# Kernel optimization log

Measured on AMD Instinct MI355X. Metric: run time of the kernel, lower is better.

## Reference

```python
import jax, jax.numpy as jnp
import numpy as np

D_FEAT = 6
T = 64
HID = 128
N = 8192
EPS = 1e-5


def setup_inputs() -> dict:
    key = jax.random.key(0)
    ks = jax.random.split(key, 16)
    s = 0.08
    rn = lambda k, shape: jax.random.normal(k, shape, dtype=jnp.float32) * s
    return {
        "x": jax.random.normal(ks[0], (N, D_FEAT * T), dtype=jnp.float32),
        "w_ih0": rn(ks[1], (3 * HID, D_FEAT)),
        "w_hh0": rn(ks[2], (3 * HID, HID)),
        "b_ih0": rn(ks[3], (3 * HID,)),
        "b_hh0": rn(ks[4], (3 * HID,)),
        "w_ih1": rn(ks[5], (3 * HID, HID)),
        "w_hh1": rn(ks[6], (3 * HID, HID)),
        "b_ih1": rn(ks[7], (3 * HID,)),
        "b_hh1": rn(ks[8], (3 * HID,)),
        "bn1_g": jnp.ones((HID,), jnp.float32),
        "bn1_b": jnp.zeros((HID,), jnp.float32),
        "fc_w": rn(ks[9], (HID, HID)),
        "fc_b": rn(ks[10], (HID,)),
        "bn2_g": jnp.ones((HID,), jnp.float32),
        "bn2_b": jnp.zeros((HID,), jnp.float32),
        "fco_w": rn(ks[11], (1, HID)),
        "fco_b": rn(ks[12], (1,)),
    }


def _gru_layer(xs, w_ih, w_hh, b_ih, b_hh):
    # xs: [T, N, in] -> per-step hidden states [T, N, H] (torch nn.GRU math)
    H = w_hh.shape[1]
    gi_all = jnp.einsum('tni,gi->tng', xs, w_ih) + b_ih  # precompute input gates [T,N,3H]

    def step(h, gi):
        gh = h @ w_hh.T + b_hh
        i_r, i_z, i_n = jnp.split(gi, 3, axis=1)
        h_r, h_z, h_n = jnp.split(gh, 3, axis=1)
        r = jax.nn.sigmoid(i_r + h_r)
        z = jax.nn.sigmoid(i_z + h_z)
        n = jnp.tanh(i_n + r * h_n)
        h_new = (1.0 - z) * n + z * h
        return h_new, h_new

    h0 = jnp.zeros((xs.shape[1], H), dtype=xs.dtype)
    _, hs = jax.lax.scan(step, h0, gi_all)
    return hs


def _bn(x, g, b):
    # BatchNorm1d with track_running_stats=False: always uses batch stats
    mu = jnp.mean(x, axis=0)
    var = jnp.mean((x - mu) ** 2, axis=0)
    return (x - mu) * jax.lax.rsqrt(var + EPS) * g + b


def reference(x, w_ih0, w_hh0, b_ih0, b_hh0, w_ih1, w_hh1, b_ih1, b_hh1,
              bn1_g, bn1_b, fc_w, fc_b, bn2_g, bn2_b, fco_w, fco_b):
    n = x.shape[0]
    # reshape(N, d_feat, T).permute(0,2,1) -> time-major [T, N, d_feat] for scan
    xs = x.reshape(n, D_FEAT, T).transpose(2, 0, 1)
    h1 = _gru_layer(xs, w_ih0, w_hh0, b_ih0, b_hh0)
    h2 = _gru_layer(h1, w_ih1, w_hh1, b_ih1, b_hh1)
    hidden = _bn(h2[-1], bn1_g, bn1_b)  # [N, H]
    # cal_attention: mean_d(h_i * h_j) - mean(h_i)*mean(h_j)
    #   == (hidden @ hidden.T)/H - outer(row_means, row_means)  (exact identity)
    m = jnp.mean(hidden, axis=1)
    att = hidden @ hidden.T / jnp.float32(hidden.shape[1]) - jnp.outer(m, m)  # [N, N]
    out = att @ hidden              # [N, H]
    out = out @ fc_w.T + fc_b
    out = _bn(out, bn2_g, bn2_b)
    out = jax.nn.leaky_relu(out, 0.01)
    return (out @ fco_w.T + fco_b).squeeze(-1)  # [N]
```

## Files before the change

### kernel.cpp

```cpp
#include <hip/hip_runtime.h>

typedef unsigned short u16;
typedef short bf16x8 __attribute__((ext_vector_type(8)));
typedef float f32x4 __attribute__((ext_vector_type(4)));

#define NBATCH 8192

__device__ __forceinline__ f32x4 mfma16(bf16x8 a, bf16x8 b, f32x4 c) {
  return __builtin_amdgcn_mfma_f32_16x16x32_bf16(a, b, c, 0, 0, 0);
}
__device__ __forceinline__ u16 f2bf(float f) {
  unsigned int u = __float_as_uint(f);
  return (u16)((u + 0x7FFFu + ((u >> 16) & 1u)) >> 16);
}
__device__ __forceinline__ float bf2f(u16 h) {
  return __uint_as_float(((unsigned int)h) << 16);
}
__device__ __forceinline__ float sigm(float x) {
  return __builtin_amdgcn_rcpf(1.f + __builtin_amdgcn_exp2f(-1.44269504f * x));
}
__device__ __forceinline__ float tanh_(float x) {
  float t = __builtin_amdgcn_exp2f(2.88539008f * x);
  return 1.f - 2.f * __builtin_amdgcn_rcpf(t + 1.f);
}
__device__ __forceinline__ bf16x8 pack8(const float* p) {
  float4 a = *(const float4*)p, b = *(const float4*)(p + 4);
  bf16x8 r;
  r[0] = (short)f2bf(a.x); r[1] = (short)f2bf(a.y);
  r[2] = (short)f2bf(a.z); r[3] = (short)f2bf(a.w);
  r[4] = (short)f2bf(b.x); r[5] = (short)f2bf(b.y);
  r[6] = (short)f2bf(b.z); r[7] = (short)f2bf(b.w);
  return r;
}

#define WHH0_OFF 0
#define H0B_OFF  98304
#define H1B_OFF  114688
#define XB_OFF   131072
#define GRU_LDS  135168

#define GRU_STEP(RD, WR, T)                                                     \
  {                                                                             \
    if (xact && (T) < 63) {                                                     \
      u16 xh = f2bf(xv);                                                        \
      u16 xl = f2bf(xv - bf2f(xh));                                             \
      char* xw = sm + XB_OFF + (WR)*2048 + xm*64 + xd*2;                        \
      *(u16*)xw = xh; *(u16*)(xw + 16) = xl; *(u16*)(xw + 32) = xh;             \
      if ((T) < 62) xv = gx[(T) + 2];                                           \
    }                                                                           \
    f32x4 rz0[2][2], hn0[2], in0[2];                                            \
    _Pragma("unroll") for (int mt = 0; mt < 2; ++mt) {                          \
      rz0[mt][0] = (f32x4){brz0r, brz0r, brz0r, brz0r};                         \
      rz0[mt][1] = (f32x4){brz0z, brz0z, brz0z, brz0z};                         \
      hn0[mt] = (f32x4){bhn0, bhn0, bhn0, bhn0};                                \
      in0[mt] = (f32x4){bin0, bin0, bin0, bin0};                                \
    }                                                                           \
    _Pragma("unroll") for (int ki = 0; ki < 4; ++ki) {                          \
      bf16x8 a0 = *(bf16x8*)(sm + H0B_OFF + (RD)*8192 + arow0 + ad[ki]);        \
      bf16x8 a1 = *(bf16x8*)(sm + H0B_OFF + (RD)*8192 + arow1 + ad[ki]);        \
      bf16x8 b0 = *(bf16x8*)(sm + brow0 + ad[ki]);                              \
      bf16x8 b1 = *(bf16x8*)(sm + brow1 + ad[ki]);                              \
      bf16x8 b2 = *(bf16x8*)(sm + brow2 + ad[ki]);                              \
      rz0[0][0] = mfma16(a0, b0, rz0[0][0]);                                    \
      rz0[0][1] = mfma16(a0, b1, rz0[0][1]);                                    \
      hn0[0]    = mfma16(a0, b2, hn0[0]);                                       \
      rz0[1][0] = mfma16(a1, b0, rz0[1][0]);                                    \
      rz0[1][1] = mfma16(a1, b1, rz0[1][1]);                                    \
      hn0[1]    = mfma16(a1, b2, hn0[1]);                                       \
    }                                                                           \
    {                                                                           \
      bf16x8 ax0 = *(bf16x8*)(sm + XB_OFF + (RD)*2048 + xr0);                   \
      bf16x8 ax1 = *(bf16x8*)(sm + XB_OFF + (RD)*2048 + xr1);                   \
      rz0[0][0] = mfma16(ax0, wf0a, rz0[0][0]);                                 \
      rz0[0][1] = mfma16(ax0, wf0b, rz0[0][1]);                                 \
      in0[0]    = mfma16(ax0, wf0c, in0[0]);                                    \
      rz0[1][0] = mfma16(ax1, wf0a, rz0[1][0]);                                 \
      rz0[1][1] = mfma16(ax1, wf0b, rz0[1][1]);                                 \
      in0[1]    = mfma16(ax1, wf0c, in0[1]);                                    \
    }                                                                           \
    _Pragma("unroll") for (int mt = 0; mt < 2; ++mt)                            \
    _Pragma("unroll") for (int r = 0; r < 4; ++r) {                             \
      int s = mt*4 + r;                                                         \
      float rr = sigm(rz0[mt][0][r]);                                           \
      float zz = sigm(rz0[mt][1][r]);                                           \
      float nn = tanh_(__builtin_fmaf(rr, hn0[mt][r], in0[mt][r]));             \
      float h = h0s[s]; h = __builtin_fmaf(zz, h - nn, nn); h0s[s] = h;         \
      *(u16*)(sm + H0B_OFF + (WR)*8192 + st[s]) = f2bf(h);                      \
    }                                                                           \
    __syncthreads();                                                            \
    f32x4 rz1[2][2], hn1[2], in1[2];                                            \
    _Pragma("unroll") for (int mt = 0; mt < 2; ++mt) {                          \
      rz1[mt][0] = (f32x4){brz1r, brz1r, brz1r, brz1r};                         \
      rz1[mt][1] = (f32x4){brz1z, brz1z, brz1z, brz1z};                         \
      hn1[mt] = (f32x4){bhn1, bhn1, bhn1, bhn1};                                \
      in1[mt] = (f32x4){bin1, bin1, bin1, bin1};                                \
    }                                                                           \
    _Pragma("unroll") for (int ki = 0; ki < 4; ++ki) {                          \
      bf16x8 p0 = *(bf16x8*)(sm + H0B_OFF + (WR)*8192 + arow0 + ad[ki]);        \
      bf16x8 p1 = *(bf16x8*)(sm + H0B_OFF + (WR)*8192 + arow1 + ad[ki]);        \
      bf16x8 q0 = *(bf16x8*)(sm + H1B_OFF + (RD)*8192 + arow0 + ad[ki]);        \
      bf16x8 q1 = *(bf16x8*)(sm + H1B_OFF + (RD)*8192 + arow1 + ad[ki]);        \
      rz1[0][0] = mfma16(p0, wih1f[0][ki], rz1[0][0]);                          \
      rz1[0][0] = mfma16(q0, whh1f[0][ki], rz1[0][0]);                          \
      rz1[0][1] = mfma16(p0, wih1f[1][ki], rz1[0][1]);                          \
      rz1[0][1] = mfma16(q0, whh1f[1][ki], rz1[0][1]);                          \
      in1[0]    = mfma16(p0, wih1f[2][ki], in1[0]);                             \
      hn1[0]    = mfma16(q0, whh1f[2][ki], hn1[0]);                             \
      rz1[1][0] = mfma16(p1, wih1f[0][ki], rz1[1][0]);                          \
      rz1[1][0] = mfma16(q1, whh1f[0][ki], rz1[1][0]);                          \
      rz1[1][1] = mfma16(p1, wih1f[1][ki], rz1[1][1]);                          \
      rz1[1][1] = mfma16(q1, whh1f[1][ki], rz1[1][1]);                          \
      in1[1]    = mfma16(p1, wih1f[2][ki], in1[1]);                             \
      hn1[1]    = mfma16(q1, whh1f[2][ki], hn1[1]);                             \
    }                                                                           \
    _Pragma("unroll") for (int mt = 0; mt < 2; ++mt)                            \
    _Pragma("unroll") for (int r = 0; r < 4; ++r) {                             \
      int s = mt*4 + r;                                                         \
      float rr = sigm(rz1[mt][0][r]);                                           \
      float zz = sigm(rz1[mt][1][r]);                                           \
      float nn = tanh_(__builtin_fmaf(rr, hn1[mt][r], in1[mt][r]));             \
      float h = h1s[s]; h = __builtin_fmaf(zz, h - nn, nn); h1s[s] = h;         \
      *(u16*)(sm + H1B_OFF + (WR)*8192 + st[s]) = f2bf(h);                      \
    }                                                                           \
  }

__global__ __attribute__((amdgpu_flat_work_group_size(512, 512), amdgpu_waves_per_eu(2, 2)))
void k_gru(const float* __restrict__ x,
           const float* __restrict__ wih0, const float* __restrict__ whh0,
           const float* __restrict__ bih0, const float* __restrict__ bhh0,
           const float* __restrict__ wih1, const float* __restrict__ whh1,
           const float* __restrict__ bih1, const float* __restrict__ bhh1,
           float* __restrict__ hraw) {
  extern __shared__ char sm[];
  const int tid = threadIdx.x;
  const int wid = tid >> 6;
  const int lane = tid & 63;
  const int lq = lane >> 4;
  const int ul = lane & 15;
  const int u  = wid * 16 + ul;
  const int n0 = blockIdx.x * 32;
  const int sx = (ul & 7) << 4;

  for (int idx = tid; idx < 9216; idx += 512)
    *(float*)(sm + H0B_OFF + idx * 4) = 0.f;
  for (int idx = tid; idx < 12288; idx += 512) {
    int g = idx >> 5, c4 = (idx & 31) * 4;
    float4 v = *(const float4*)(whh0 + g * 128 + c4);
    unsigned int p0 = (unsigned int)f2bf(v.x) | ((unsigned int)f2bf(v.y) << 16);
    unsigned int p1 = (unsigned int)f2bf(v.z) | ((unsigned int)f2bf(v.w) << 16);
    unsigned int* dst = (unsigned int*)(sm + WHH0_OFF + g * 256 + ((c4 * 2) ^ ((g & 7) << 4)));
    dst[0] = p0; dst[1] = p1;
  }

  bf16x8 wih1f[3][4], whh1f[3][4];
#pragma unroll
  for (int i = 0; i < 3; ++i) {
    int g = u + 128 * i;
#pragma unroll
    for (int ki = 0; ki < 4; ++ki) {
      wih1f[i][ki] = pack8(wih1 + g * 128 + ki * 32 + lq * 8);
      whh1f[i][ki] = pack8(whh1 + g * 128 + ki * 32 + lq * 8);
    }
  }
  bf16x8 wf0a, wf0b, wf0c;
  {
    u16 t0[8] = {0,0,0,0,0,0,0,0}, t1[8] = {0,0,0,0,0,0,0,0}, t2[8] = {0,0,0,0,0,0,0,0};
    u16* ts[3] = {t0, t1, t2};
#pragma unroll
    for (int i = 0; i < 3; ++i) {
      int g = u + 128 * i;
      if (lq < 2) {
        for (int d = 0; d < 6; ++d) ts[i][d] = f2bf(wih0[g * 6 + d]);
      } else if (lq == 2) {
        for (int d = 0; d < 6; ++d) {
          float w = wih0[g * 6 + d];
          u16 h = f2bf(w);
          ts[i][d] = f2bf(w - bf2f(h));
        }
      }
    }
    wf0a = *(bf16x8*)t0; wf0b = *(bf16x8*)t1; wf0c = *(bf16x8*)t2;
  }
  const float brz0r = bih0[u] + bhh0[u];
  const float brz0z = bih0[u + 128] + bhh0[u + 128];
  const float bin0 = bih0[u + 256], bhn0 = bhh0[u + 256];
  const float brz1r = bih1[u] + bhh1[u];
  const float brz1z = bih1[u + 128] + bhh1[u + 128];
  const float bin1 = bih1[u + 256], bhn1 = bhh1[u + 256];

  int ad[4];
#pragma unroll
  for (int ki = 0; ki < 4; ++ki) ad[ki] = (ki * 64 + lq * 16) ^ sx;
  const int arow0 = ul * 256, arow1 = arow0 + 4096;
  const int xr0 = ul * 64 + lq * 16, xr1 = xr0 + 1024;
  const int brow0 = WHH0_OFF + u * 256;
  const int brow1 = WHH0_OFF + (u + 128) * 256;
  const int brow2 = WHH0_OFF + (u + 256) * 256;
  int st[8];
#pragma unroll
  for (int mt = 0; mt < 2; ++mt)
#pragma unroll
    for (int r = 0; r < 4; ++r) {
      int m = mt * 16 + lq * 4 + r;
      st[mt * 4 + r] = m * 256 + ((u * 2) ^ ((m & 7) << 4));
    }

  float h0s[8], h1s[8];
#pragma unroll
  for (int s = 0; s < 8; ++s) { h0s[s] = 0.f; h1s[s] = 0.f; }

  const int xm = tid / 6, xd = tid - 6 * xm;
  const bool xact = tid < 192;
  const float* gx = x + (size_t)(n0 + xm) * 384 + xd * 64;

  __syncthreads();

  float xv = 0.f;
  if (xact) {
    float x0 = gx[0];
    u16 h = f2bf(x0);
    u16 l = f2bf(x0 - bf2f(h));
    char* p = sm + XB_OFF + xm * 64 + xd * 2;
    *(u16*)p = h; *(u16*)(p + 16) = l; *(u16*)(p + 32) = h;
    xv = gx[1];
  }
  __syncthreads();

  for (int t = 0; t < 64; t += 2) {
    GRU_STEP(0, 1, t)
    GRU_STEP(1, 0, t + 1)
  }

#pragma unroll
  for (int mt = 0; mt < 2; ++mt)
#pragma unroll
    for (int r = 0; r < 4; ++r) {
      int m = mt * 16 + lq * 4 + r;
      hraw[(size_t)(n0 + m) * 128 + u] = h1s[mt * 4 + r];
    }
}

__global__ void k_bn1p(const float* __restrict__ hraw, float* __restrict__ p) {
  __shared__ float s0[256], s1[256];
  int tid = threadIdx.x, b = blockIdx.x;
  int f = tid & 127, r = tid >> 7;
  float s = 0.f, q = 0.f;
  for (int n = b * 64 + r; n < b * 64 + 64; n += 2) {
    float v = hraw[(size_t)n * 128 + f];
    s += v; q += v * v;
  }
  s0[tid] = s; s1[tid] = q;
  __syncthreads();
  if (tid < 128) {
    p[b * 256 + tid] = s0[tid] + s0[tid + 128];
    p[b * 256 + 128 + tid] = s1[tid] + s1[tid + 128];
  }
}

__global__ void k_bn1r(const float* __restrict__ p, float* __restrict__ mu1,
                       float* __restrict__ rs1) {
  int f = threadIdx.x;
  float s = 0.f, q = 0.f;
  for (int b = 0; b < 128; ++b) { s += p[b * 256 + f]; q += p[b * 256 + 128 + f]; }
  float mu = s / 8192.f, var = q / 8192.f - mu * mu;
  mu1[f] = mu; rs1[f] = rsqrtf(var + 1e-5f);
}

__global__ void k_attp(const float* __restrict__ hraw, const float* __restrict__ mu1,
                       const float* __restrict__ rs1, const float* __restrict__ g1,
                       const float* __restrict__ b1, float* __restrict__ hidden,
                       float* __restrict__ mvec, float* __restrict__ gpart,
                       float* __restrict__ mhpart) {
  __shared__ float hid[64][128];
  __shared__ float mld[64];
  int tid = threadIdx.x, blk = blockIdx.x, n0 = blk * 64;
  for (int idx = tid; idx < 64 * 128; idx += 256) {
    int n = idx >> 7, f = idx & 127;
    float v = (hraw[(size_t)(n0 + n) * 128 + f] - mu1[f]) * rs1[f] * g1[f] + b1[f];
    hid[n][f] = v;
    hidden[(size_t)(n0 + n) * 128 + f] = v;
  }
  __syncthreads();
  if (tid < 64) {
    float s = 0.f;
    for (int f = 0; f < 128; ++f) s += hid[tid][f];
    s *= (1.f / 128.f);
    mld[tid] = s; mvec[n0 + tid] = s;
  }
  __syncthreads();
  int i = tid >> 1, j0 = (tid & 1) * 64;
  float acc[64];
#pragma unroll
  for (int j = 0; j < 64; ++j) acc[j] = 0.f;
  for (int n = 0; n < 64; ++n) {
    float a = hid[n][i];
#pragma unroll
    for (int j = 0; j < 64; ++j) acc[j] += a * hid[n][j0 + j];
  }
#pragma unroll
  for (int j = 0; j < 64; ++j) gpart[(size_t)blk * 16384 + i * 128 + j0 + j] = acc[j];
  if (tid < 128) {
    float s = 0.f;
    for (int n = 0; n < 64; ++n) s += mld[n] * hid[n][tid];
    mhpart[blk * 128 + tid] = s;
  }
}

__global__ void k_attfa(const float* __restrict__ gpart, const float* __restrict__ mhpart,
                        float* __restrict__ gfull, float* __restrict__ mhfull) {
  int idx = blockIdx.x * 256 + threadIdx.x;
  float s = 0.f;
  for (int b = 0; b < 128; ++b) s += gpart[(size_t)b * 16384 + idx];
  gfull[idx] = s;
  if (blockIdx.x == 0 && threadIdx.x < 128) {
    float t = 0.f;
    for (int b = 0; b < 128; ++b) t += mhpart[b * 128 + threadIdx.x];
    mhfull[threadIdx.x] = t;
  }
}

__global__ void k_attfb(const float* __restrict__ gfull, const float* __restrict__ mhfull,
                        const float* __restrict__ fcw, float* __restrict__ m2,
                        float* __restrict__ uvec) {
  int idx = blockIdx.x * 128 + threadIdx.x;
  int k = idx >> 7, j = idx & 127;
  const float4* ga = (const float4*)(gfull + k * 128);
  const float4* fb = (const float4*)(fcw + j * 128);
  float a0 = 0.f, a1 = 0.f, a2 = 0.f, a3 = 0.f;
#pragma unroll 8
  for (int f = 0; f < 32; ++f) {
    float4 a = ga[f], b = fb[f];
    a0 += a.x * b.x; a1 += a.y * b.y; a2 += a.z * b.z; a3 += a.w * b.w;
  }
  m2[idx] = (a0 + a1 + a2 + a3) * (1.f / 128.f);
  if (idx < 128) {
    float s = 0.f;
    const float* fr = fcw + idx * 128;
#pragma unroll 8
    for (int f = 0; f < 128; ++f) s += mhfull[f] * fr[f];
    uvec[idx] = s;
  }
}

__global__ void k_out2(const float* __restrict__ hidden, const float* __restrict__ mvec,
                       const float* __restrict__ m2g, const float* __restrict__ uvec,
                       const float* __restrict__ fcb, float* __restrict__ out2,
                       float* __restrict__ bn2p) {
  extern __shared__ char smo[];
  float* m2l = (float*)smo;
  float* hl = m2l + 16384;
  float* ml = hl + 4096;
  float* red = ml + 32;
  int tid = threadIdx.x, blk = blockIdx.x, n0 = blk * 32;
  for (int idx = tid; idx < 16384; idx += 256) m2l[idx] = m2g[idx];
  for (int idx = tid; idx < 4096; idx += 256) hl[idx] = hidden[(size_t)n0 * 128 + idx];
  if (tid < 32) ml[tid] = mvec[n0 + tid];
  __syncthreads();
  int j = tid & 127, rg = tid >> 7;
  float uj = uvec[j], bj = fcb[j];
  float s1 = 0.f, s2 = 0.f;
  for (int q = 0; q < 16; ++q) {
    int nl = rg * 16 + q;
    float s = bj - ml[nl] * uj;
    const float* hr = hl + nl * 128;
#pragma unroll 8
    for (int k = 0; k < 128; ++k) s += hr[k] * m2l[k * 128 + j];
    out2[(size_t)(n0 + nl) * 128 + j] = s;
    s1 += s; s2 += s * s;
  }
  red[tid] = s1; red[256 + tid] = s2;
  __syncthreads();
  if (tid < 128) {
    bn2p[blk * 256 + tid] = red[tid] + red[128 + tid];
    bn2p[blk * 256 + 128 + tid] = red[256 + tid] + red[384 + tid];
  }
}

__global__ void k_bn2(const float* __restrict__ bn2p, float* __restrict__ mu2,
                      float* __restrict__ rs2) {
  int j = threadIdx.x;
  float s = 0.f, q = 0.f;
  for (int b = 0; b < 256; ++b) {
    s += bn2p[b * 256 + j];
    q += bn2p[b * 256 + 128 + j];
  }
  float mu = s / 8192.f, var = q / 8192.f - mu * mu;
  mu2[j] = mu; rs2[j] = rsqrtf(var + 1e-5f);
}

__global__ void k_fin(const float* __restrict__ out2, const float* __restrict__ mu2,
                      const float* __restrict__ rs2, const float* __restrict__ g2,
                      const float* __restrict__ b2, const float* __restrict__ fcow,
                      const float* __restrict__ fcob, float* __restrict__ y) {
  int tid = threadIdx.x, lane = tid & 63, w = tid >> 6;
  int n = blockIdx.x * 4 + w;
  float s = 0.f;
#pragma unroll
  for (int h = 0; h < 2; ++h) {
    int j = lane + h * 64;
    float v = (out2[(size_t)n * 128 + j] - mu2[j]) * rs2[j] * g2[j] + b2[j];
    v = fmaxf(v, 0.01f * v);
    s += v * fcow[j];
  }
  for (int off = 32; off; off >>= 1) s += __shfl_down(s, off);
  if (!lane) y[n] = s + fcob[0];
}

extern "C" void kernel_launch(void* const* d_in, const int* in_sizes, int n_in,
                              void* d_out, int out_size, void* d_ws, size_t ws_size,
                              hipStream_t stream) {
  const float* x    = (const float*)d_in[0];
  const float* wih0 = (const float*)d_in[1];
  const float* whh0 = (const float*)d_in[2];
  const float* bih0 = (const float*)d_in[3];
  const float* bhh0 = (const float*)d_in[4];
  const float* wih1 = (const float*)d_in[5];
  const float* whh1 = (const float*)d_in[6];
  const float* bih1 = (const float*)d_in[7];
  const float* bhh1 = (const float*)d_in[8];
  const float* g1   = (const float*)d_in[9];
  const float* b1   = (const float*)d_in[10];
  const float* fcw  = (const float*)d_in[11];
  const float* fcb  = (const float*)d_in[12];
  const float* g2   = (const float*)d_in[13];
  const float* b2   = (const float*)d_in[14];
  const float* fcow = (const float*)d_in[15];
  const float* fcob = (const float*)d_in[16];

  char* ws = (char*)d_ws;
  float* hraw   = (float*)(ws + 0);
  float* hidden = (float*)(ws + 4194304);
  float* mvec   = (float*)(ws + 8388608);
  float* mu1    = (float*)(ws + 8421376);
  float* rs1    = (float*)(ws + 8421888);
  float* gpart  = (float*)(ws + 8422400);
  float* mhpart = (float*)(ws + 16811008);
  float* m2     = (float*)(ws + 16876544);
  float* uvec   = (float*)(ws + 16942080);
  float* out2   = (float*)(ws + 16942592);
  float* bn2p   = (float*)(ws + 21136896);
  float* mu2    = (float*)(ws + 21399040);
  float* rs2    = (float*)(ws + 21399552);
  float* gfull  = (float*)(ws + 21400064);
  float* mhfull = (float*)(ws + 21465600);

  (void)hipFuncSetAttribute((const void*)k_gru,
                            hipFuncAttributeMaxDynamicSharedMemorySize, GRU_LDS);
  (void)hipFuncSetAttribute((const void*)k_out2,
                            hipFuncAttributeMaxDynamicSharedMemorySize, 84096);

  k_gru<<<256, 512, GRU_LDS, stream>>>(x, wih0, whh0, bih0, bhh0, wih1, whh1,
                                       bih1, bhh1, hraw);
  k_bn1p<<<128, 256, 0, stream>>>(hraw, bn2p);
  k_bn1r<<<1, 128, 0, stream>>>(bn2p, mu1, rs1);
  k_attp<<<128, 256, 0, stream>>>(hraw, mu1, rs1, g1, b1, hidden, mvec, gpart, mhpart);
  k_attfa<<<64, 256, 0, stream>>>(gpart, mhpart, gfull, mhfull);
  k_attfb<<<128, 128, 0, stream>>>(gfull, mhfull, fcw, m2, uvec);
  k_out2<<<256, 256, 84096, stream>>>(hidden, mvec, m2, uvec, fcb, out2, bn2p);
  k_bn2<<<1, 128, 0, stream>>>(bn2p, mu2, rs2);
  k_fin<<<2048, 256, 0, stream>>>(out2, mu2, rs2, g2, b2, fcow, fcob, (float*)d_out);
}
```

Before: 312.4 us.

## Split fused two-layer GRU kernel into separate per-layer kernels via global h0 sequence

The fused GRU kernel, which ran both layers per timestep with layer-1 input and recurrent weights held in registers, is split into two kernels. k_gru0 runs layer 0 and streams each step's bf16 hidden state to a global buffer (16 MB in total). k_gru1 keeps W_hh1 in LDS and W_ih1 in registers, prefetching the next step's h0 from global while it computes. This frees registers and drops the waves_per_eu constraint, which could raise occupancy and shorten each kernel's serial chain. In exchange it adds global write and read traffic plus a second serial 64-step pass, and the two layers can no longer overlap.

After: 335.0 us. 7.2% more time.

```diff
diff --git a/kernel.cpp b/kernel.cpp
--- a/kernel.cpp
+++ b/kernel.cpp
@@ -33,18 +33,18 @@
   return r;
 }
 
-#define WHH0_OFF 0
-#define H0B_OFF  98304
-#define H1B_OFF  114688
-#define XB_OFF   131072
-#define GRU_LDS  135168
-
-#define GRU_STEP(RD, WR, T)                                                     \
+
+#define A_WHH0 0
+#define A_H0B  98304
+#define A_XB   114688
+#define A_LDS  118784
+
+#define GRU0_STEP(RD, WR, T)                                                    \
   {                                                                             \
     if (xact && (T) < 63) {                                                     \
       u16 xh = f2bf(xv);                                                        \
       u16 xl = f2bf(xv - bf2f(xh));                                             \
-      char* xw = sm + XB_OFF + (WR)*2048 + xm*64 + xd*2;                        \
+      char* xw = sm + A_XB + (WR)*2048 + xm*64 + xd*2;                          \
       *(u16*)xw = xh; *(u16*)(xw + 16) = xl; *(u16*)(xw + 32) = xh;             \
       if ((T) < 62) xv = gx[(T) + 2];                                           \
     }                                                                           \
@@ -56,8 +56,8 @@
       in0[mt] = (f32x4){bin0, bin0, bin0, bin0};                                \
     }                                                                           \
     _Pragma("unroll") for (int ki = 0; ki < 4; ++ki) {                          \
-      bf16x8 a0 = *(bf16x8*)(sm + H0B_OFF + (RD)*8192 + arow0 + ad[ki]);        \
-      bf16x8 a1 = *(bf16x8*)(sm + H0B_OFF + (RD)*8192 + arow1 + ad[ki]);        \
+      bf16x8 a0 = *(bf16x8*)(sm + A_H0B + (RD)*8192 + arow0 + ad[ki]);          \
+      bf16x8 a1 = *(bf16x8*)(sm + A_H0B + (RD)*8192 + arow1 + ad[ki]);          \
       bf16x8 b0 = *(bf16x8*)(sm + brow0 + ad[ki]);                              \
       bf16x8 b1 = *(bf16x8*)(sm + brow1 + ad[ki]);                              \
       bf16x8 b2 = *(bf16x8*)(sm + brow2 + ad[ki]);                              \
@@ -69,14 +69,18 @@
       hn0[1]    = mfma16(a1, b2, hn0[1]);                                       \
     }                                                                           \
     {                                                                           \
-      bf16x8 ax0 = *(bf16x8*)(sm + XB_OFF + (RD)*2048 + xr0);                   \
-      bf16x8 ax1 = *(bf16x8*)(sm + XB_OFF + (RD)*2048 + xr1);                   \
+      bf16x8 ax0 = *(bf16x8*)(sm + A_XB + (RD)*2048 + xr0);                     \
+      bf16x8 ax1 = *(bf16x8*)(sm + A_XB + (RD)*2048 + xr1);                     \
       rz0[0][0] = mfma16(ax0, wf0a, rz0[0][0]);                                 \
       rz0[0][1] = mfma16(ax0, wf0b, rz0[0][1]);                                 \
       in0[0]    = mfma16(ax0, wf0c, in0[0]);                                    \
       rz0[1][0] = mfma16(ax1, wf0a, rz0[1][0]);                                 \
       rz0[1][1] = mfma16(ax1, wf0b, rz0[1][1]);                                 \
       in0[1]    = mfma16(ax1, wf0c, in0[1]);                                    \
+    }                                                                           \
+    if ((T) >= 1) {       \
+      uint4 gv = *(const uint4*)(sm + A_H0B + (RD)*8192 + tid*16);              \
+      *(uint4*)(h0seq + (size_t)((T)-1)*2097152 + gofs) = gv;                   \
     }                                                                           \
     _Pragma("unroll") for (int mt = 0; mt < 2; ++mt)                            \
     _Pragma("unroll") for (int r = 0; r < 4; ++r) {                             \
@@ -85,52 +89,16 @@
       float zz = sigm(rz0[mt][1][r]);                                           \
       float nn = tanh_(__builtin_fmaf(rr, hn0[mt][r], in0[mt][r]));             \
       float h = h0s[s]; h = __builtin_fmaf(zz, h - nn, nn); h0s[s] = h;         \
-      *(u16*)(sm + H0B_OFF + (WR)*8192 + st[s]) = f2bf(h);                      \
+      *(u16*)(sm + A_H0B + (WR)*8192 + st[s]) = f2bf(h);                        \
     }                                                                           \
     __syncthreads();                                                            \
-    f32x4 rz1[2][2], hn1[2], in1[2];                                            \
-    _Pragma("unroll") for (int mt = 0; mt < 2; ++mt) {                          \
-      rz1[mt][0] = (f32x4){brz1r, brz1r, brz1r, brz1r};                         \
-      rz1[mt][1] = (f32x4){brz1z, brz1z, brz1z, brz1z};                         \
-      hn1[mt] = (f32x4){bhn1, bhn1, bhn1, bhn1};                                \
-      in1[mt] = (f32x4){bin1, bin1, bin1, bin1};                                \
-    }                                                                           \
-    _Pragma("unroll") for (int ki = 0; ki < 4; ++ki) {                          \
-      bf16x8 p0 = *(bf16x8*)(sm + H0B_OFF + (WR)*8192 + arow0 + ad[ki]);        \
-      bf16x8 p1 = *(bf16x8*)(sm + H0B_OFF + (WR)*8192 + arow1 + ad[ki]);        \
-      bf16x8 q0 = *(bf16x8*)(sm + H1B_OFF + (RD)*8192 + arow0 + ad[ki]);        \
-      bf16x8 q1 = *(bf16x8*)(sm + H1B_OFF + (RD)*8192 + arow1 + ad[ki]);        \
-      rz1[0][0] = mfma16(p0, wih1f[0][ki], rz1[0][0]);                          \
-      rz1[0][0] = mfma16(q0, whh1f[0][ki], rz1[0][0]);                          \
-      rz1[0][1] = mfma16(p0, wih1f[1][ki], rz1[0][1]);                          \
-      rz1[0][1] = mfma16(q0, whh1f[1][ki], rz1[0][1]);                          \
-      in1[0]    = mfma16(p0, wih1f[2][ki], in1[0]);                             \
-      hn1[0]    = mfma16(q0, whh1f[2][ki], hn1[0]);                             \
-      rz1[1][0] = mfma16(p1, wih1f[0][ki], rz1[1][0]);                          \
-      rz1[1][0] = mfma16(q1, whh1f[0][ki], rz1[1][0]);                          \
-      rz1[1][1] = mfma16(p1, wih1f[1][ki], rz1[1][1]);                          \
-      rz1[1][1] = mfma16(q1, whh1f[1][ki], rz1[1][1]);                          \
-      in1[1]    = mfma16(p1, wih1f[2][ki], in1[1]);                             \
-      hn1[1]    = mfma16(q1, whh1f[2][ki], hn1[1]);                             \
-    }                                                                           \
-    _Pragma("unroll") for (int mt = 0; mt < 2; ++mt)                            \
-    _Pragma("unroll") for (int r = 0; r < 4; ++r) {                             \
-      int s = mt*4 + r;                                                         \
-      float rr = sigm(rz1[mt][0][r]);                                           \
-      float zz = sigm(rz1[mt][1][r]);                                           \
-      float nn = tanh_(__builtin_fmaf(rr, hn1[mt][r], in1[mt][r]));             \
-      float h = h1s[s]; h = __builtin_fmaf(zz, h - nn, nn); h1s[s] = h;         \
-      *(u16*)(sm + H1B_OFF + (WR)*8192 + st[s]) = f2bf(h);                      \
-    }                                                                           \
-  }
-
-__global__ __attribute__((amdgpu_flat_work_group_size(512, 512), amdgpu_waves_per_eu(2, 2)))
-void k_gru(const float* __restrict__ x,
-           const float* __restrict__ wih0, const float* __restrict__ whh0,
-           const float* __restrict__ bih0, const float* __restrict__ bhh0,
-           const float* __restrict__ wih1, const float* __restrict__ whh1,
-           const float* __restrict__ bih1, const float* __restrict__ bhh1,
-           float* __restrict__ hraw) {
+  }
+
+__global__ __attribute__((amdgpu_flat_work_group_size(512, 512)))
+void k_gru0(const float* __restrict__ x,
+            const float* __restrict__ wih0, const float* __restrict__ whh0,
+            const float* __restrict__ bih0, const float* __restrict__ bhh0,
+            char* __restrict__ h0seq) {
   extern __shared__ char sm[];
   const int tid = threadIdx.x;
   const int wid = tid >> 6;
@@ -140,28 +108,19 @@
   const int u  = wid * 16 + ul;
   const int n0 = blockIdx.x * 32;
   const int sx = (ul & 7) << 4;
-
-  for (int idx = tid; idx < 9216; idx += 512)
-    *(float*)(sm + H0B_OFF + idx * 4) = 0.f;
+  const int gofs = blockIdx.x * 8192 + tid * 16;
+
+  for (int idx = tid; idx < 5120; idx += 512)
+    *(float*)(sm + A_H0B + idx * 4) = 0.f;
   for (int idx = tid; idx < 12288; idx += 512) {
     int g = idx >> 5, c4 = (idx & 31) * 4;
     float4 v = *(const float4*)(whh0 + g * 128 + c4);
     unsigned int p0 = (unsigned int)f2bf(v.x) | ((unsigned int)f2bf(v.y) << 16);
     unsigned int p1 = (unsigned int)f2bf(v.z) | ((unsigned int)f2bf(v.w) << 16);
-    unsigned int* dst = (unsigned int*)(sm + WHH0_OFF + g * 256 + ((c4 * 2) ^ ((g & 7) << 4)));
+    unsigned int* dst = (unsigned int*)(sm + A_WHH0 + g * 256 + ((c4 * 2) ^ ((g & 7) << 4)));
     dst[0] = p0; dst[1] = p1;
   }
 
-  bf16x8 wih1f[3][4], whh1f[3][4];
-#pragma unroll
-  for (int i = 0; i < 3; ++i) {
-    int g = u + 128 * i;
-#pragma unroll
-    for (int ki = 0; ki < 4; ++ki) {
-      wih1f[i][ki] = pack8(wih1 + g * 128 + ki * 32 + lq * 8);
-      whh1f[i][ki] = pack8(whh1 + g * 128 + ki * 32 + lq * 8);
-    }
-  }
   bf16x8 wf0a, wf0b, wf0c;
   {
     u16 t0[8] = {0,0,0,0,0,0,0,0}, t1[8] = {0,0,0,0,0,0,0,0}, t2[8] = {0,0,0,0,0,0,0,0};
@@ -184,18 +143,15 @@
   const float brz0r = bih0[u] + bhh0[u];
   const float brz0z = bih0[u + 128] + bhh0[u + 128];
   const float bin0 = bih0[u + 256], bhn0 = bhh0[u + 256];
-  const float brz1r = bih1[u] + bhh1[u];
-  const float brz1z = bih1[u + 128] + bhh1[u + 128];
-  const float bin1 = bih1[u + 256], bhn1 = bhh1[u + 256];
 
   int ad[4];
 #pragma unroll
   for (int ki = 0; ki < 4; ++ki) ad[ki] = (ki * 64 + lq * 16) ^ sx;
   const int arow0 = ul * 256, arow1 = arow0 + 4096;
   const int xr0 = ul * 64 + lq * 16, xr1 = xr0 + 1024;
-  const int brow0 = WHH0_OFF + u * 256;
-  const int brow1 = WHH0_OFF + (u + 128) * 256;
-  const int brow2 = WHH0_OFF + (u + 256) * 256;
+  const int brow0 = A_WHH0 + u * 256;
+  const int brow1 = A_WHH0 + (u + 128) * 256;
+  const int brow2 = A_WHH0 + (u + 256) * 256;
   int st[8];
 #pragma unroll
   for (int mt = 0; mt < 2; ++mt)
@@ -205,9 +161,9 @@
       st[mt * 4 + r] = m * 256 + ((u * 2) ^ ((m & 7) << 4));
     }
 
-  float h0s[8], h1s[8];
-#pragma unroll
-  for (int s = 0; s < 8; ++s) { h0s[s] = 0.f; h1s[s] = 0.f; }
+  float h0s[8];
+#pragma unroll
+  for (int s = 0; s < 8; ++s) h0s[s] = 0.f;
 
   const int xm = tid / 6, xd = tid - 6 * xm;
   const bool xact = tid < 192;
@@ -220,15 +176,138 @@
     float x0 = gx[0];
     u16 h = f2bf(x0);
     u16 l = f2bf(x0 - bf2f(h));
-    char* p = sm + XB_OFF + xm * 64 + xd * 2;
+    char* p = sm + A_XB + xm * 64 + xd * 2;
     *(u16*)p = h; *(u16*)(p + 16) = l; *(u16*)(p + 32) = h;
     xv = gx[1];
   }
   __syncthreads();
 
   for (int t = 0; t < 64; t += 2) {
-    GRU_STEP(0, 1, t)
-    GRU_STEP(1, 0, t + 1)
+    GRU0_STEP(0, 1, t)
+    GRU0_STEP(1, 0, t + 1)
+  }
+  {
+    uint4 gv = *(const uint4*)(sm + A_H0B + 0 * 8192 + tid * 16);
+    *(uint4*)(h0seq + (size_t)63 * 2097152 + gofs) = gv;
+  }
+}
+
+#define B_WHH1 0
+#define B_H0IN 98304
+#define B_H1B  114688
+#define B_LDS  131072
+
+#define GRU1_STEP(RD, WR, T)                                                    \
+  {                                                                             \
+    uint4 hv = {0u, 0u, 0u, 0u};                                                \
+    if ((T) < 63) hv = *(const uint4*)(gsrc + (size_t)((T)+1)*2097152);         \
+    f32x4 rz1[2][2], hn1[2], in1[2];                                            \
+    _Pragma("unroll") for (int mt = 0; mt < 2; ++mt) {                          \
+      rz1[mt][0] = (f32x4){brz1r, brz1r, brz1r, brz1r};                         \
+      rz1[mt][1] = (f32x4){brz1z, brz1z, brz1z, brz1z};                         \
+      hn1[mt] = (f32x4){bhn1, bhn1, bhn1, bhn1};                                \
+      in1[mt] = (f32x4){bin1, bin1, bin1, bin1};                                \
+    }                                                                           \
+    _Pragma("unroll") for (int ki = 0; ki < 4; ++ki) {                          \
+      bf16x8 p0 = *(bf16x8*)(sm + B_H0IN + (RD)*8192 + arow0 + ad[ki]);         \
+      bf16x8 p1 = *(bf16x8*)(sm + B_H0IN + (RD)*8192 + arow1 + ad[ki]);         \
+      bf16x8 q0 = *(bf16x8*)(sm + B_H1B + (RD)*8192 + arow0 + ad[ki]);          \
+      bf16x8 q1 = *(bf16x8*)(sm + B_H1B + (RD)*8192 + arow1 + ad[ki]);          \
+      bf16x8 w0 = *(bf16x8*)(sm + brow0 + ad[ki]);                              \
+      bf16x8 w1 = *(bf16x8*)(sm + brow1 + ad[ki]);                              \
+      bf16x8 w2 = *(bf16x8*)(sm + brow2 + ad[ki]);                              \
+      rz1[0][0] = mfma16(p0, wih1f[0][ki], rz1[0][0]);                          \
+      rz1[0][0] = mfma16(q0, w0, rz1[0][0]);                                    \
+      rz1[0][1] = mfma16(p0, wih1f[1][ki], rz1[0][1]);                          \
+      rz1[0][1] = mfma16(q0, w1, rz1[0][1]);                                    \
+      in1[0]    = mfma16(p0, wih1f[2][ki], in1[0]);                             \
+      hn1[0]    = mfma16(q0, w2, hn1[0]);                                       \
+      rz1[1][0] = mfma16(p1, wih1f[0][ki], rz1[1][0]);                          \
+      rz1[1][0] = mfma16(q1, w0, rz1[1][0]);                                    \
+      rz1[1][1] = mfma16(p1, wih1f[1][ki], rz1[1][1]);                          \
+      rz1[1][1] = mfma16(q1, w1, rz1[1][1]);                                    \
+      in1[1]    = mfma16(p1, wih1f[2][ki], in1[1]);                             \
+      hn1[1]    = mfma16(q1, w2, hn1[1]);                                       \
+    }                                                                           \
+    if ((T) < 63) *(uint4*)(sm + B_H0IN + (WR)*8192 + tid*16) = hv;             \
+    _Pragma("unroll") for (int mt = 0; mt < 2; ++mt)                            \
+    _Pragma("unroll") for (int r = 0; r < 4; ++r) {                             \
+      int s = mt*4 + r;                                                         \
+      float rr = sigm(rz1[mt][0][r]);                                           \
+      float zz = sigm(rz1[mt][1][r]);                                           \
+      float nn = tanh_(__builtin_fmaf(rr, hn1[mt][r], in1[mt][r]));             \
+      float h = h1s[s]; h = __builtin_fmaf(zz, h - nn, nn); h1s[s] = h;         \
+      *(u16*)(sm + B_H1B + (WR)*8192 + st[s]) = f2bf(h);                        \
+    }                                                                           \
+    __syncthreads();                                                            \
+  }
+
+__global__ __attribute__((amdgpu_flat_work_group_size(512, 512)))
+void k_gru1(const float* __restrict__ wih1, const float* __restrict__ whh1,
+            const float* __restrict__ bih1, const float* __restrict__ bhh1,
+            const char* __restrict__ h0seq, float* __restrict__ hraw) {
+  extern __shared__ char sm[];
+  const int tid = threadIdx.x;
+  const int wid = tid >> 6;
+  const int lane = tid & 63;
+  const int lq = lane >> 4;
+  const int ul = lane & 15;
+  const int u  = wid * 16 + ul;
+  const int n0 = blockIdx.x * 32;
+  const int sx = (ul & 7) << 4;
+  const char* gsrc = h0seq + blockIdx.x * 8192 + tid * 16;
+
+  for (int idx = tid; idx < 2048; idx += 512)
+    *(float*)(sm + B_H1B + idx * 4) = 0.f;
+  for (int idx = tid; idx < 12288; idx += 512) {
+    int g = idx >> 5, c4 = (idx & 31) * 4;
+    float4 v = *(const float4*)(whh1 + g * 128 + c4);
+    unsigned int p0 = (unsigned int)f2bf(v.x) | ((unsigned int)f2bf(v.y) << 16);
+    unsigned int p1 = (unsigned int)f2bf(v.z) | ((unsigned int)f2bf(v.w) << 16);
+    unsigned int* dst = (unsigned int*)(sm + B_WHH1 + g * 256 + ((c4 * 2) ^ ((g & 7) << 4)));
+    dst[0] = p0; dst[1] = p1;
+  }
+  {
+    uint4 h0v = *(const uint4*)(gsrc);
+    *(uint4*)(sm + B_H0IN + tid * 16) = h0v;
+  }
+  bf16x8 wih1f[3][4];
+#pragma unroll
+  for (int i = 0; i < 3; ++i) {
+    int g = u + 128 * i;
+#pragma unroll
+    for (int ki = 0; ki < 4; ++ki)
+      wih1f[i][ki] = pack8(wih1 + g * 128 + ki * 32 + lq * 8);
+  }
+  const float brz1r = bih1[u] + bhh1[u];
+  const float brz1z = bih1[u + 128] + bhh1[u + 128];
+  const float bin1 = bih1[u + 256], bhn1 = bhh1[u + 256];
+
+  int ad[4];
+#pragma unroll
+  for (int ki = 0; ki < 4; ++ki) ad[ki] = (ki * 64 + lq * 16) ^ sx;
+  const int arow0 = ul * 256, arow1 = arow0 + 4096;
+  const int brow0 = B_WHH1 + u * 256;
+  const int brow1 = B_WHH1 + (u + 128) * 256;
+  const int brow2 = B_WHH1 + (u + 256) * 256;
+  int st[8];
+#pragma unroll
+  for (int mt = 0; mt < 2; ++mt)
+#pragma unroll
+    for (int r = 0; r < 4; ++r) {
+      int m = mt * 16 + lq * 4 + r;
+      st[mt * 4 + r] = m * 256 + ((u * 2) ^ ((m & 7) << 4));
+    }
+
+  float h1s[8];
+#pragma unroll
+  for (int s = 0; s < 8; ++s) h1s[s] = 0.f;
+
+  __syncthreads();
+
+  for (int t = 0; t < 64; t += 2) {
+    GRU1_STEP(0, 1, t)
+    GRU1_STEP(1, 0, t + 1)
   }
 
 #pragma unroll
@@ -443,14 +522,17 @@
   float* rs2    = (float*)(ws + 21399552);
   float* gfull  = (float*)(ws + 21400064);
   float* mhfull = (float*)(ws + 21465600);
-
-  (void)hipFuncSetAttribute((const void*)k_gru,
-                            hipFuncAttributeMaxDynamicSharedMemorySize, GRU_LDS);
+  char*  h0seq  = (char*)(ws + 21495808);
+
+  (void)hipFuncSetAttribute((const void*)k_gru0,
+                            hipFuncAttributeMaxDynamicSharedMemorySize, A_LDS);
+  (void)hipFuncSetAttribute((const void*)k_gru1,
+                            hipFuncAttributeMaxDynamicSharedMemorySize, B_LDS);
   (void)hipFuncSetAttribute((const void*)k_out2,
                             hipFuncAttributeMaxDynamicSharedMemorySize, 84096);
 
-  k_gru<<<256, 512, GRU_LDS, stream>>>(x, wih0, whh0, bih0, bhh0, wih1, whh1,
-                                       bih1, bhh1, hraw);
+  k_gru0<<<256, 512, A_LDS, stream>>>(x, wih0, whh0, bih0, bhh0, h0seq);
+  k_gru1<<<256, 512, B_LDS, stream>>>(wih1, whh1, bih1, bhh1, h0seq, hraw);
   k_bn1p<<<128, 256, 0, stream>>>(hraw, bn2p);
   k_bn1r<<<1, 128, 0, stream>>>(bn2p, mu1, rs1);
   k_attp<<<128, 256, 0, stream>>>(hraw, mu1, rs1, g1, b1, hidden, mvec, gpart, mhpart);
```

## Wavefront-pipeline GRU layers across separate wave groups in a 1024-thread block

Applied to the files above, without the earlier changes.

The GRU kernel now runs layer 0 and layer 1 on separate groups of 8 waves in a 1024-thread block. Layer 1 processes step k-1 while layer 0 processes step k, so each timestep needs one barrier instead of two serialized layer phases. Register-resident weight fragments now hold whh0 for layer 0 or wih1 for layer 1, and whh1 moves to LDS. Each step carries one extra iteration for the pipeline skew. Doubling the threads per block raises register pressure and drops the previous waves-per-EU hint.

New measurement: 625.2 us. 100% more time.

```diff
diff --git a/kernel.cpp b/kernel.cpp
--- a/kernel.cpp
+++ b/kernel.cpp
@@ -33,98 +33,80 @@
   return r;
 }
 
-#define WHH0_OFF 0
-#define H0B_OFF  98304
-#define H1B_OFF  114688
-#define XB_OFF   131072
-#define GRU_LDS  135168
-
-#define GRU_STEP(RD, WR, T)                                                     \
+#define W1_OFF 0
+#define H0B_OFF 98304
+#define H1B_OFF 114688
+#define XB_OFF  131072
+#define GRU_LDS 135168
+
+#define FITER(P, K)                                                             \
   {                                                                             \
-    if (xact && (T) < 63) {                                                     \
+    if (xact && (K) < 63) {                                                     \
       u16 xh = f2bf(xv);                                                        \
       u16 xl = f2bf(xv - bf2f(xh));                                             \
-      char* xw = sm + XB_OFF + (WR)*2048 + xm*64 + xd*2;                        \
+      char* xw = sm + XB_OFF + ((P)^1)*2048 + xm*64 + xd*2;                     \
       *(u16*)xw = xh; *(u16*)(xw + 16) = xl; *(u16*)(xw + 32) = xh;             \
-      if ((T) < 62) xv = gx[(T) + 2];                                           \
+      if ((K) < 62) xv = gx[(K) + 2];                                           \
     }                                                                           \
-    f32x4 rz0[2][2], hn0[2], in0[2];                                            \
-    _Pragma("unroll") for (int mt = 0; mt < 2; ++mt) {                          \
-      rz0[mt][0] = (f32x4){brz0r, brz0r, brz0r, brz0r};                         \
-      rz0[mt][1] = (f32x4){brz0z, brz0z, brz0z, brz0z};                         \
-      hn0[mt] = (f32x4){bhn0, bhn0, bhn0, bhn0};                                \
-      in0[mt] = (f32x4){bin0, bin0, bin0, bin0};                                \
-    }                                                                           \
-    _Pragma("unroll") for (int ki = 0; ki < 4; ++ki) {                          \
-      bf16x8 a0 = *(bf16x8*)(sm + H0B_OFF + (RD)*8192 + arow0 + ad[ki]);        \
-      bf16x8 a1 = *(bf16x8*)(sm + H0B_OFF + (RD)*8192 + arow1 + ad[ki]);        \
-      bf16x8 b0 = *(bf16x8*)(sm + brow0 + ad[ki]);                              \
-      bf16x8 b1 = *(bf16x8*)(sm + brow1 + ad[ki]);                              \
-      bf16x8 b2 = *(bf16x8*)(sm + brow2 + ad[ki]);                              \
-      rz0[0][0] = mfma16(a0, b0, rz0[0][0]);                                    \
-      rz0[0][1] = mfma16(a0, b1, rz0[0][1]);                                    \
-      hn0[0]    = mfma16(a0, b2, hn0[0]);                                       \
-      rz0[1][0] = mfma16(a1, b0, rz0[1][0]);                                    \
-      rz0[1][1] = mfma16(a1, b1, rz0[1][1]);                                    \
-      hn0[1]    = mfma16(a1, b2, hn0[1]);                                       \
-    }                                                                           \
-    {                                                                           \
-      bf16x8 ax0 = *(bf16x8*)(sm + XB_OFF + (RD)*2048 + xr0);                   \
-      bf16x8 ax1 = *(bf16x8*)(sm + XB_OFF + (RD)*2048 + xr1);                   \
-      rz0[0][0] = mfma16(ax0, wf0a, rz0[0][0]);                                 \
-      rz0[0][1] = mfma16(ax0, wf0b, rz0[0][1]);                                 \
-      in0[0]    = mfma16(ax0, wf0c, in0[0]);                                    \
-      rz0[1][0] = mfma16(ax1, wf0a, rz0[1][0]);                                 \
-      rz0[1][1] = mfma16(ax1, wf0b, rz0[1][1]);                                 \
-      in0[1]    = mfma16(ax1, wf0c, in0[1]);                                    \
-    }                                                                           \
-    _Pragma("unroll") for (int mt = 0; mt < 2; ++mt)                            \
-    _Pragma("unroll") for (int r = 0; r < 4; ++r) {                             \
-      int s = mt*4 + r;                                                         \
-      float rr = sigm(rz0[mt][0][r]);                                           \
-      float zz = sigm(rz0[mt][1][r]);                                           \
-      float nn = tanh_(__builtin_fmaf(rr, hn0[mt][r], in0[mt][r]));             \
-      float h = h0s[s]; h = __builtin_fmaf(zz, h - nn, nn); h0s[s] = h;         \
-      *(u16*)(sm + H0B_OFF + (WR)*8192 + st[s]) = f2bf(h);                      \
+    if (isL0 ? ((K) < 64) : ((K) >= 1)) {                                       \
+      f32x4 rzr[2], rzz[2], cc[2], dd[2];                                       \
+      _Pragma("unroll") for (int mt = 0; mt < 2; ++mt) {                        \
+        rzr[mt] = (f32x4){brzr, brzr, brzr, brzr};                              \
+        rzz[mt] = (f32x4){brzz, brzz, brzz, brzz};                              \
+        cc[mt]  = (f32x4){bcc, bcc, bcc, bcc};                                  \
+        dd[mt]  = (f32x4){bdd, bdd, bdd, bdd};                                  \
+      }                                                                         \
+      _Pragma("unroll") for (int ki = 0; ki < 4; ++ki) {                        \
+        bf16x8 a0 = *(bf16x8*)(sm + H0B_OFF + ((P)^1)*8192 + arow0 + ad[ki]);   \
+        bf16x8 a1 = *(bf16x8*)(sm + H0B_OFF + ((P)^1)*8192 + arow1 + ad[ki]);   \
+        rzr[0] = mfma16(a0, wfrag[0][ki], rzr[0]);                              \
+        rzr[1] = mfma16(a1, wfrag[0][ki], rzr[1]);                              \
+        rzz[0] = mfma16(a0, wfrag[1][ki], rzz[0]);                              \
+        rzz[1] = mfma16(a1, wfrag[1][ki], rzz[1]);                              \
+        cc[0]  = mfma16(a0, wfrag[2][ki], cc[0]);                               \
+        cc[1]  = mfma16(a1, wfrag[2][ki], cc[1]);                               \
+      }                                                                         \
+      if (isL0) {                                                               \
+        bf16x8 ax0 = *(bf16x8*)(sm + XB_OFF + (P)*2048 + xr0);                  \
+        bf16x8 ax1 = *(bf16x8*)(sm + XB_OFF + (P)*2048 + xr1);                  \
+        rzr[0] = mfma16(ax0, wf0a, rzr[0]);                                     \
+        rzr[1] = mfma16(ax1, wf0a, rzr[1]);                                     \
+        rzz[0] = mfma16(ax0, wf0b, rzz[0]);                                     \
+        rzz[1] = mfma16(ax1, wf0b, rzz[1]);                                     \
+        dd[0]  = mfma16(ax0, wf0c, dd[0]);                                      \
+        dd[1]  = mfma16(ax1, wf0c, dd[1]);                                      \
+      } else {                                                                  \
+        _Pragma("unroll") for (int ki = 0; ki < 4; ++ki) {                      \
+          bf16x8 q0 = *(bf16x8*)(sm + H1B_OFF + (P)*8192 + arow0 + ad[ki]);     \
+          bf16x8 q1 = *(bf16x8*)(sm + H1B_OFF + (P)*8192 + arow1 + ad[ki]);     \
+          bf16x8 w0 = *(bf16x8*)(sm + W1_OFF + brow0 + ad[ki]);                 \
+          bf16x8 w1 = *(bf16x8*)(sm + W1_OFF + brow1 + ad[ki]);                 \
+          bf16x8 w2 = *(bf16x8*)(sm + W1_OFF + brow2 + ad[ki]);                 \
+          rzr[0] = mfma16(q0, w0, rzr[0]);                                      \
+          rzr[1] = mfma16(q1, w0, rzr[1]);                                      \
+          rzz[0] = mfma16(q0, w1, rzz[0]);                                      \
+          rzz[1] = mfma16(q1, w1, rzz[1]);                                      \
+          dd[0]  = mfma16(q0, w2, dd[0]);                                       \
+          dd[1]  = mfma16(q1, w2, dd[1]);                                       \
+        }                                                                       \
+      }                                                                         \
+      const int wbase = (P) ? wb1 : wb0;                                        \
+      _Pragma("unroll") for (int mt = 0; mt < 2; ++mt)                          \
+      _Pragma("unroll") for (int r = 0; r < 4; ++r) {                           \
+        int s = mt*4 + r;                                                       \
+        float rr = sigm(rzr[mt][r]);                                            \
+        float zz = sigm(rzz[mt][r]);                                            \
+        float iv = isL0 ? dd[mt][r] : cc[mt][r];                                \
+        float hv = isL0 ? cc[mt][r] : dd[mt][r];                                \
+        float nn = tanh_(__builtin_fmaf(rr, hv, iv));                           \
+        float h = hs[s]; h = __builtin_fmaf(zz, h - nn, nn); hs[s] = h;         \
+        *(u16*)(sm + wbase + st[s]) = f2bf(h);                                  \
+      }                                                                         \
     }                                                                           \
     __syncthreads();                                                            \
-    f32x4 rz1[2][2], hn1[2], in1[2];                                            \
-    _Pragma("unroll") for (int mt = 0; mt < 2; ++mt) {                          \
-      rz1[mt][0] = (f32x4){brz1r, brz1r, brz1r, brz1r};                         \
-      rz1[mt][1] = (f32x4){brz1z, brz1z, brz1z, brz1z};                         \
-      hn1[mt] = (f32x4){bhn1, bhn1, bhn1, bhn1};                                \
-      in1[mt] = (f32x4){bin1, bin1, bin1, bin1};                                \
-    }                                                                           \
-    _Pragma("unroll") for (int ki = 0; ki < 4; ++ki) {                          \
-      bf16x8 p0 = *(bf16x8*)(sm + H0B_OFF + (WR)*8192 + arow0 + ad[ki]);        \
-      bf16x8 p1 = *(bf16x8*)(sm + H0B_OFF + (WR)*8192 + arow1 + ad[ki]);        \
-      bf16x8 q0 = *(bf16x8*)(sm + H1B_OFF + (RD)*8192 + arow0 + ad[ki]);        \
-      bf16x8 q1 = *(bf16x8*)(sm + H1B_OFF + (RD)*8192 + arow1 + ad[ki]);        \
-      rz1[0][0] = mfma16(p0, wih1f[0][ki], rz1[0][0]);                          \
-      rz1[0][0] = mfma16(q0, whh1f[0][ki], rz1[0][0]);                          \
-      rz1[0][1] = mfma16(p0, wih1f[1][ki], rz1[0][1]);                          \
-      rz1[0][1] = mfma16(q0, whh1f[1][ki], rz1[0][1]);                          \
-      in1[0]    = mfma16(p0, wih1f[2][ki], in1[0]);                             \
-      hn1[0]    = mfma16(q0, whh1f[2][ki], hn1[0]);                             \
-      rz1[1][0] = mfma16(p1, wih1f[0][ki], rz1[1][0]);                          \
-      rz1[1][0] = mfma16(q1, whh1f[0][ki], rz1[1][0]);                          \
-      rz1[1][1] = mfma16(p1, wih1f[1][ki], rz1[1][1]);                          \
-      rz1[1][1] = mfma16(q1, whh1f[1][ki], rz1[1][1]);                          \
-      in1[1]    = mfma16(p1, wih1f[2][ki], in1[1]);                             \
-      hn1[1]    = mfma16(q1, whh1f[2][ki], hn1[1]);                             \
-    }                                                                           \
-    _Pragma("unroll") for (int mt = 0; mt < 2; ++mt)                            \
-    _Pragma("unroll") for (int r = 0; r < 4; ++r) {                             \
-      int s = mt*4 + r;                                                         \
-      float rr = sigm(rz1[mt][0][r]);                                           \
-      float zz = sigm(rz1[mt][1][r]);                                           \
-      float nn = tanh_(__builtin_fmaf(rr, hn1[mt][r], in1[mt][r]));             \
-      float h = h1s[s]; h = __builtin_fmaf(zz, h - nn, nn); h1s[s] = h;         \
-      *(u16*)(sm + H1B_OFF + (WR)*8192 + st[s]) = f2bf(h);                      \
-    }                                                                           \
-  }
-
-__global__ __attribute__((amdgpu_flat_work_group_size(512, 512), amdgpu_waves_per_eu(2, 2)))
+  }
+
+__global__ __attribute__((amdgpu_flat_work_group_size(1024, 1024)))
 void k_gru(const float* __restrict__ x,
            const float* __restrict__ wih0, const float* __restrict__ whh0,
            const float* __restrict__ bih0, const float* __restrict__ bhh0,
@@ -134,33 +116,33 @@
   extern __shared__ char sm[];
   const int tid = threadIdx.x;
   const int wid = tid >> 6;
+  const bool isL0 = wid < 8;
   const int lane = tid & 63;
   const int lq = lane >> 4;
   const int ul = lane & 15;
-  const int u  = wid * 16 + ul;
+  const int u  = (wid & 7) * 16 + ul;
   const int n0 = blockIdx.x * 32;
   const int sx = (ul & 7) << 4;
 
-  for (int idx = tid; idx < 9216; idx += 512)
+  for (int idx = tid; idx < 9216; idx += 1024)
     *(float*)(sm + H0B_OFF + idx * 4) = 0.f;
-  for (int idx = tid; idx < 12288; idx += 512) {
+  for (int idx = tid; idx < 12288; idx += 1024) {
     int g = idx >> 5, c4 = (idx & 31) * 4;
-    float4 v = *(const float4*)(whh0 + g * 128 + c4);
+    float4 v = *(const float4*)(whh1 + g * 128 + c4);
     unsigned int p0 = (unsigned int)f2bf(v.x) | ((unsigned int)f2bf(v.y) << 16);
     unsigned int p1 = (unsigned int)f2bf(v.z) | ((unsigned int)f2bf(v.w) << 16);
-    unsigned int* dst = (unsigned int*)(sm + WHH0_OFF + g * 256 + ((c4 * 2) ^ ((g & 7) << 4)));
+    unsigned int* dst = (unsigned int*)(sm + W1_OFF + g * 256 + ((c4 * 2) ^ ((g & 7) << 4)));
     dst[0] = p0; dst[1] = p1;
   }
 
-  bf16x8 wih1f[3][4], whh1f[3][4];
+  const float* wsrc = isL0 ? whh0 : wih1;
+  bf16x8 wfrag[3][4];
 #pragma unroll
   for (int i = 0; i < 3; ++i) {
     int g = u + 128 * i;
 #pragma unroll
-    for (int ki = 0; ki < 4; ++ki) {
-      wih1f[i][ki] = pack8(wih1 + g * 128 + ki * 32 + lq * 8);
-      whh1f[i][ki] = pack8(whh1 + g * 128 + ki * 32 + lq * 8);
-    }
+    for (int ki = 0; ki < 4; ++ki)
+      wfrag[i][ki] = pack8(wsrc + g * 128 + ki * 32 + lq * 8);
   }
   bf16x8 wf0a, wf0b, wf0c;
   {
@@ -181,21 +163,19 @@
     }
     wf0a = *(bf16x8*)t0; wf0b = *(bf16x8*)t1; wf0c = *(bf16x8*)t2;
   }
-  const float brz0r = bih0[u] + bhh0[u];
-  const float brz0z = bih0[u + 128] + bhh0[u + 128];
-  const float bin0 = bih0[u + 256], bhn0 = bhh0[u + 256];
-  const float brz1r = bih1[u] + bhh1[u];
-  const float brz1z = bih1[u + 128] + bhh1[u + 128];
-  const float bin1 = bih1[u + 256], bhn1 = bhh1[u + 256];
+  const float brzr = isL0 ? (bih0[u] + bhh0[u]) : (bih1[u] + bhh1[u]);
+  const float brzz = isL0 ? (bih0[u + 128] + bhh0[u + 128]) : (bih1[u + 128] + bhh1[u + 128]);
+  const float bcc  = isL0 ? bhh0[u + 256] : bih1[u + 256];
+  const float bdd  = isL0 ? bih0[u + 256] : bhh1[u + 256];
 
   int ad[4];
 #pragma unroll
   for (int ki = 0; ki < 4; ++ki) ad[ki] = (ki * 64 + lq * 16) ^ sx;
   const int arow0 = ul * 256, arow1 = arow0 + 4096;
   const int xr0 = ul * 64 + lq * 16, xr1 = xr0 + 1024;
-  const int brow0 = WHH0_OFF + u * 256;
-  const int brow1 = WHH0_OFF + (u + 128) * 256;
-  const int brow2 = WHH0_OFF + (u + 256) * 256;
+  const int brow0 = u * 256;
+  const int brow1 = (u + 128) * 256;
+  const int brow2 = (u + 256) * 256;
   int st[8];
 #pragma unroll
   for (int mt = 0; mt < 2; ++mt)
@@ -204,10 +184,12 @@
       int m = mt * 16 + lq * 4 + r;
       st[mt * 4 + r] = m * 256 + ((u * 2) ^ ((m & 7) << 4));
     }
-
-  float h0s[8], h1s[8];
-#pragma unroll
-  for (int s = 0; s < 8; ++s) { h0s[s] = 0.f; h1s[s] = 0.f; }
+  const int wb0 = isL0 ? (H0B_OFF + 0)    : (H1B_OFF + 8192);
+  const int wb1 = isL0 ? (H0B_OFF + 8192) : (H1B_OFF + 0);
+
+  float hs[8];
+#pragma unroll
+  for (int s = 0; s < 8; ++s) hs[s] = 0.f;
 
   const int xm = tid / 6, xd = tid - 6 * xm;
   const bool xact = tid < 192;
@@ -226,18 +208,21 @@
   }
   __syncthreads();
 
-  for (int t = 0; t < 64; t += 2) {
-    GRU_STEP(0, 1, t)
-    GRU_STEP(1, 0, t + 1)
-  }
-
-#pragma unroll
-  for (int mt = 0; mt < 2; ++mt)
-#pragma unroll
-    for (int r = 0; r < 4; ++r) {
-      int m = mt * 16 + lq * 4 + r;
-      hraw[(size_t)(n0 + m) * 128 + u] = h1s[mt * 4 + r];
-    }
+  for (int k = 0; k < 64; k += 2) {
+    FITER(0, k)
+    FITER(1, k + 1)
+  }
+  FITER(0, 64)
+
+  if (!isL0) {
+#pragma unroll
+    for (int mt = 0; mt < 2; ++mt)
+#pragma unroll
+      for (int r = 0; r < 4; ++r) {
+        int m = mt * 16 + lq * 4 + r;
+        hraw[(size_t)(n0 + m) * 128 + u] = hs[mt * 4 + r];
+      }
+  }
 }
 
 __global__ void k_bn1p(const float* __restrict__ hraw, float* __restrict__ p) {
@@ -449,8 +434,8 @@
   (void)hipFuncSetAttribute((const void*)k_out2,
                             hipFuncAttributeMaxDynamicSharedMemorySize, 84096);
 
-  k_gru<<<256, 512, GRU_LDS, stream>>>(x, wih0, whh0, bih0, bhh0, wih1, whh1,
-                                       bih1, bhh1, hraw);
+  k_gru<<<256, 1024, GRU_LDS, stream>>>(x, wih0, whh0, bih0, bhh0, wih1, whh1,
+                                        bih1, bhh1, hraw);
   k_bn1p<<<128, 256, 0, stream>>>(hraw, bn2p);
   k_bn1r<<<1, 128, 0, stream>>>(bn2p, mu1, rs1);
   k_attp<<<128, 256, 0, stream>>>(hraw, mu1, rs1, g1, b1, hidden, mvec, gpart, mhpart);
```
